# Kernel optimization log

Hardware: AMD Instinct MI355X
Metric: run time of the kernel (lower is better)

## Reference

```python
import jax, jax.numpy as jnp
import numpy as np

INPUT_SIZE = 256
HIDDEN_SIZE = 256


def _xavier(key, shape):
    fan_in, fan_out = shape
    limit = float(np.sqrt(6.0 / (fan_in + fan_out)))
    return jax.random.uniform(key, shape, jnp.float32, -limit, limit)


def setup_inputs() -> dict:
    key = jax.random.key(0)
    ks = jax.random.split(key, 9)
    X = jax.random.normal(ks[0], (64, 2048, INPUT_SIZE), jnp.float32)
    E, H = INPUT_SIZE, HIDDEN_SIZE
    return {
        "X": X,
        "W_ii": _xavier(ks[1], (E, H)), "W_hi": _xavier(ks[2], (H, H)), "b_i": jnp.zeros((H,), jnp.float32),
        "W_if": _xavier(ks[3], (E, H)), "W_hf": _xavier(ks[4], (H, H)), "b_f": jnp.zeros((H,), jnp.float32),
        "W_ig": _xavier(ks[5], (E, H)), "W_hg": _xavier(ks[6], (H, H)), "b_g": jnp.zeros((H,), jnp.float32),
        "W_io": _xavier(ks[7], (E, H)), "W_ho": _xavier(ks[8], (H, H)), "b_o": jnp.zeros((H,), jnp.float32),
    }


def reference(X, W_ii, W_hi, b_i, W_if, W_hf, b_f, W_ig, W_hg, b_g, W_io, W_ho, b_o):
    B, S, E = X.shape
    H = W_ii.shape[1]
    h0 = jnp.zeros((B, H), X.dtype)  # init state in torch code is zeros (broadcasts to (B,H))
    c0 = jnp.zeros((B, H), X.dtype)

    def step(carry, x_t):
        h, c = carry
        i = jax.nn.sigmoid(x_t @ W_ii + h @ W_hi + b_i)
        f = jax.nn.sigmoid(x_t @ W_if + h @ W_hf + b_f)
        g = jnp.tanh(x_t @ W_ig + h @ W_hg + b_g)
        o = jax.nn.sigmoid(x_t @ W_io + h @ W_ho + b_o)
        c = f * c + i * g
        h = o * jnp.tanh(c)
        return (h, c), h

    (h_t, c_t), hs = jax.lax.scan(step, (h0, c0), jnp.swapaxes(X, 0, 1))  # hs: (S,B,H)
    hiddenSeqs = jnp.swapaxes(hs, 0, 1)  # (B,S,H)
    return hiddenSeqs, (h_t, c_t)
```

## Files before the change

### kernel.cpp

```cpp
#include <hip/hip_runtime.h>

typedef _Float16 f16;
typedef _Float16 f16x2 __attribute__((ext_vector_type(2)));
typedef _Float16 f16x8 __attribute__((ext_vector_type(8)));
typedef float    f32x4 __attribute__((ext_vector_type(4)));
typedef unsigned int u32x4 __attribute__((ext_vector_type(4)));

#if defined(__has_builtin)
#if __has_builtin(__builtin_amdgcn_fdot2)
#define HAVE_FDOT2 1
#endif
#endif

#ifdef HAVE_FDOT2
#define FDOT2(a, b, c) __builtin_amdgcn_fdot2((a), (b), (c), false)
#else
static __device__ __forceinline__ float FDOT2(f16x2 a, f16x2 b, float c) {
  return c + (float)a[0] * (float)b[0] + (float)a[1] * (float)b[1];
}
#endif

static __device__ __forceinline__ f16x2 asf16x2(unsigned int v) {
  return __builtin_bit_cast(f16x2, v);
}

struct PtrPack { const float* p[8]; };

__global__ __launch_bounds__(256) void k_prep(PtrPack pp, f16* __restrict__ wxT,
                                              f16* __restrict__ whT) {
  int m = blockIdx.z, kt = blockIdx.y, ut = blockIdx.x;
  const float* src = pp.p[m];
  f16* dst = (m < 4) ? (wxT + m * 65536) : (whT + (m - 4) * 65536);
  __shared__ f16 tile[64][66];
  int c = threadIdx.x & 63, r0 = threadIdx.x >> 6;
#pragma unroll
  for (int i = 0; i < 16; ++i) {
    int r = i * 4 + r0;
    tile[c][r] = (f16)src[(kt * 64 + r) * 256 + ut * 64 + c];
  }
  __syncthreads();
#pragma unroll
  for (int i = 0; i < 16; ++i) {
    int ul = i * 4 + r0;
    dst[(size_t)(ut * 64 + ul) * 256 + kt * 64 + c] = tile[ul][c];
  }
}

__global__ __launch_bounds__(256) void k_gemm(const float* __restrict__ X,
                                              const f16* __restrict__ wxT,
                                              f16* __restrict__ xw, int chunk0) {
  int nblk = blockIdx.x;
  int mblk = blockIdx.y;
  int b    = blockIdx.z;
  __shared__ f16 Alds[64][48];
  __shared__ f16 Blds[256][48];
  int tid = threadIdx.x, wave = tid >> 6, lane = tid & 63;
  int l15 = lane & 15, l4 = lane >> 4;
  f32x4 acc[16];
#pragma unroll
  for (int i = 0; i < 16; ++i) acc[i] = (f32x4){0.f, 0.f, 0.f, 0.f};
  const float* Xb = X + ((size_t)b * 2048 + chunk0 + mblk * 64) * 256;
  const f16*   Bb = wxT + (size_t)nblk * 256 * 256;
  int arow = tid >> 2, akq = (tid & 3) * 8;

  for (int kk = 0; kk < 8; ++kk) {
    {
      const float* s = Xb + arow * 256 + kk * 32 + akq;
      float4 v0 = *(const float4*)s;
      float4 v1 = *(const float4*)(s + 4);
      union { f16 h[8]; uint4 q; } u;
      u.h[0] = (f16)v0.x; u.h[1] = (f16)v0.y; u.h[2] = (f16)v0.z; u.h[3] = (f16)v0.w;
      u.h[4] = (f16)v1.x; u.h[5] = (f16)v1.y; u.h[6] = (f16)v1.z; u.h[7] = (f16)v1.w;
      *(uint4*)(&Alds[arow][akq]) = u.q;
    }
    {
      const uint4* s = (const uint4*)(Bb + (size_t)tid * 256 + kk * 32);
      uint4* d = (uint4*)(&Blds[tid][0]);
      d[0] = s[0]; d[1] = s[1]; d[2] = s[2]; d[3] = s[3];
    }
    __syncthreads();
    f16x8 a = *(const f16x8*)(&Alds[wave * 16 + l15][l4 * 8]);
#pragma unroll
    for (int nt = 0; nt < 16; ++nt) {
      f16x8 bb = *(const f16x8*)(&Blds[nt * 16 + l15][l4 * 8]);
      acc[nt] = __builtin_amdgcn_mfma_f32_16x16x32_f16(a, bb, acc[nt], 0, 0, 0);
    }
    __syncthreads();
  }
#pragma unroll
  for (int nt = 0; nt < 16; ++nt) {
#pragma unroll
    for (int r = 0; r < 4; ++r) {
      int trow = mblk * 64 + wave * 16 + l4 * 4 + r;
      int col  = nblk * 256 + nt * 16 + l15;
      xw[((size_t)trow * 64 + b) * 1024 + col] = (f16)acc[nt][r];
    }
  }
}

__global__ __launch_bounds__(512, 2) void k_rnn(
    const f16* __restrict__ xw, const f16* __restrict__ whT,
    const float* __restrict__ bi, const float* __restrict__ bf_,
    const float* __restrict__ bg, const float* __restrict__ bo,
    float* __restrict__ out, float* __restrict__ hstate, float* __restrict__ cstate,
    int chunk0, int chunk_len) {
  extern __shared__ char smem[];
  u32x4* WO = (u32x4*)smem;
  float4* psum = (float4*)(smem + 131072);
  unsigned short* hb = (unsigned short*)(smem + 135168);
  int b = blockIdx.x;
  int u = threadIdx.x & 255;
  int half = threadIdx.x >> 8;

  const u32x4* wo = (const u32x4*)(whT + (size_t)(3 * 256 + u) * 256 + half * 128);
#pragma unroll
  for (int j = 0; j < 16; ++j) WO[(half * 16 + j) * 256 + u] = wo[j];

  const volatile u32x4* wi =
      (const volatile u32x4*)(whT + (size_t)(0 * 256 + u) * 256 + half * 128);
  const volatile u32x4* wf =
      (const volatile u32x4*)(whT + (size_t)(1 * 256 + u) * 256 + half * 128);
  const volatile u32x4* wg =
      (const volatile u32x4*)(whT + (size_t)(2 * 256 + u) * 256 + half * 128);
  u32x4 Wi[16], Wf[16], Wg[16];
#pragma unroll
  for (int j = 0; j < 16; ++j) { Wi[j] = wi[j]; Wf[j] = wf[j]; Wg[j] = wg[j]; }

  float B0 = bi[u], B1 = bf_[u], B2 = bg[u], B3 = bo[u];

  float c, h;
  if (chunk0 == 0) { c = 0.f; h = 0.f; }
  else { c = cstate[b * 256 + u]; h = hstate[b * 256 + u]; }
  if (!half) hb[u] = __builtin_bit_cast(unsigned short, (f16)h);
  __syncthreads();

  int p = 0;
#pragma unroll 1
  for (int t = 0; t < chunk_len; ++t) {
    float x0 = 0.f, x1 = 0.f, x2 = 0.f, x3 = 0.f;
    if (!half) {
      const f16* xwt = xw + ((size_t)t * 64 + b) * 1024 + u;
      x0 = (float)xwt[0]; x1 = (float)xwt[256]; x2 = (float)xwt[512]; x3 = (float)xwt[768];
    }
    const u32x4* hq = (const u32x4*)(hb + p * 256) + half * 16;
    float a0 = 0.f, a1 = 0.f, a2 = 0.f, a3 = 0.f;
#pragma unroll
    for (int j = 0; j < 16; ++j) {
      u32x4 h4 = hq[j];
      u32x4 w3 = WO[(half * 16 + j) * 256 + u];
      a0 = FDOT2(asf16x2(h4.x), asf16x2(Wi[j].x), a0);
      a1 = FDOT2(asf16x2(h4.x), asf16x2(Wf[j].x), a1);
      a2 = FDOT2(asf16x2(h4.x), asf16x2(Wg[j].x), a2);
      a3 = FDOT2(asf16x2(h4.x), asf16x2(w3.x), a3);
      a0 = FDOT2(asf16x2(h4.y), asf16x2(Wi[j].y), a0);
      a1 = FDOT2(asf16x2(h4.y), asf16x2(Wf[j].y), a1);
      a2 = FDOT2(asf16x2(h4.y), asf16x2(Wg[j].y), a2);
      a3 = FDOT2(asf16x2(h4.y), asf16x2(w3.y), a3);
      a0 = FDOT2(asf16x2(h4.z), asf16x2(Wi[j].z), a0);
      a1 = FDOT2(asf16x2(h4.z), asf16x2(Wf[j].z), a1);
      a2 = FDOT2(asf16x2(h4.z), asf16x2(Wg[j].z), a2);
      a3 = FDOT2(asf16x2(h4.z), asf16x2(w3.z), a3);
      a0 = FDOT2(asf16x2(h4.w), asf16x2(Wi[j].w), a0);
      a1 = FDOT2(asf16x2(h4.w), asf16x2(Wf[j].w), a1);
      a2 = FDOT2(asf16x2(h4.w), asf16x2(Wg[j].w), a2);
      a3 = FDOT2(asf16x2(h4.w), asf16x2(w3.w), a3);
    }
    if (half) {
      psum[u] = (float4){a0, a1, a2, a3};
    }
    __syncthreads();
    if (!half) {
      float4 ps = psum[u];
      a0 += ps.x + x0 + B0;
      a1 += ps.y + x1 + B1;
      a2 += ps.z + x2 + B2;
      a3 += ps.w + x3 + B3;
      float gi = 1.f / (1.f + __expf(-a0));
      float gf = 1.f / (1.f + __expf(-a1));
      float e2 = __expf(-2.f * fabsf(a2));
      float gg = copysignf((1.f - e2) / (1.f + e2), a2);
      float go = 1.f / (1.f + __expf(-a3));
      c = gf * c + gi * gg;
      float ec = __expf(-2.f * fabsf(c));
      float tc = copysignf((1.f - ec) / (1.f + ec), c);
      h = go * tc;
      int gt = chunk0 + t;
      out[((size_t)b * 2048 + gt) * 256 + u] = h;
      hb[(p ^ 1) * 256 + u] = __builtin_bit_cast(unsigned short, (f16)h);
      if (gt == 2047) {
        out[33554432 + b * 256 + u] = h;
        out[33554432 + 16384 + b * 256 + u] = c;
      }
    }
    __syncthreads();
    p ^= 1;
  }
  if ((chunk0 + chunk_len < 2048) && !half) {
    hstate[b * 256 + u] = h;
    cstate[b * 256 + u] = c;
  }
}

extern "C" void kernel_launch(void* const* d_in, const int* in_sizes, int n_in,
                              void* d_out, int out_size, void* d_ws, size_t ws_size,
                              hipStream_t stream) {
  const float* X = (const float*)d_in[0];
  PtrPack pp;
  pp.p[0] = (const float*)d_in[1];
  pp.p[1] = (const float*)d_in[4];
  pp.p[2] = (const float*)d_in[7];
  pp.p[3] = (const float*)d_in[10];
  pp.p[4] = (const float*)d_in[2];
  pp.p[5] = (const float*)d_in[5];
  pp.p[6] = (const float*)d_in[8];
  pp.p[7] = (const float*)d_in[11];
  const float* bi  = (const float*)d_in[3];
  const float* bf_ = (const float*)d_in[6];
  const float* bg  = (const float*)d_in[9];
  const float* bo  = (const float*)d_in[12];
  float* out = (float*)d_out;

  char* ws = (char*)d_ws;
  f16*   wxT    = (f16*)ws;
  f16*   whT    = (f16*)(ws + 524288);
  float* hstate = (float*)(ws + 1048576);
  float* cstate = (float*)(ws + 1114112);
  f16*   xwbuf  = (f16*)(ws + 1179648);

  long avail = (ws_size > 1310720) ? (long)(ws_size - 1310720) : 0;
  long sc = avail / 131072;
  sc = (sc / 64) * 64;
  if (sc < 64) sc = 64;
  if (sc > 2048) sc = 2048;

  static const int RNN_SMEM = 131072 + 4096 + 1024;
  hipFuncSetAttribute((const void*)k_rnn, hipFuncAttributeMaxDynamicSharedMemorySize,
                      RNN_SMEM);

  k_prep<<<dim3(4, 4, 8), 256, 0, stream>>>(pp, wxT, whT);

  for (int s0 = 0; s0 < 2048; s0 += (int)sc) {
    int len = (int)((2048 - s0) < sc ? (2048 - s0) : sc);
    k_gemm<<<dim3(4, len / 64, 64), 256, 0, stream>>>(X, wxT, xwbuf, s0);
    k_rnn<<<dim3(64), 512, RNN_SMEM, stream>>>(xwbuf, whT, bi, bf_, bg, bo, out,
                                               hstate, cstate, s0, len);
  }
}
```

Baseline: 3.326 ms.

## Stream input and forget gate recurrent weights from L2 instead of registers

Adds a prep kernel that stores the recurrent weights in an interleaved layout, so that each thread's 16-byte chunks for consecutive j are 256 elements apart and loads coalesce across threads. The recurrent kernel now keeps only the g-gate weights in registers and the o-gate weights in LDS. The i and f weights are reloaded from global memory (expected to hit L2) on every timestep. The goal is to cut register pressure and allow more occupancy or better scheduling, at the cost of two global loads per inner iteration on the serial critical path.

```diff
diff --git a/kernel.cpp b/kernel.cpp
--- a/kernel.cpp
+++ b/kernel.cpp
@@ -26,11 +26,10 @@
 
 struct PtrPack { const float* p[8]; };
 
-__global__ __launch_bounds__(256) void k_prep(PtrPack pp, f16* __restrict__ wxT,
-                                              f16* __restrict__ whT) {
+__global__ __launch_bounds__(256) void k_prep(PtrPack pp, f16* __restrict__ wxT) {
   int m = blockIdx.z, kt = blockIdx.y, ut = blockIdx.x;
   const float* src = pp.p[m];
-  f16* dst = (m < 4) ? (wxT + m * 65536) : (whT + (m - 4) * 65536);
+  f16* dst = wxT + m * 65536;
   __shared__ f16 tile[64][66];
   int c = threadIdx.x & 63, r0 = threadIdx.x >> 6;
 #pragma unroll
@@ -43,6 +42,23 @@
   for (int i = 0; i < 16; ++i) {
     int ul = i * 4 + r0;
     dst[(size_t)(ut * 64 + ul) * 256 + kt * 64 + c] = tile[ul][c];
+  }
+}
+
+__global__ __launch_bounds__(256) void k_prepI(PtrPack pp, u32x4* __restrict__ whI) {
+  int kb = blockIdx.x;
+  int m  = blockIdx.y;
+  const float* src = pp.p[4 + m];
+  int u = threadIdx.x;
+  f16 v[64];
+#pragma unroll
+  for (int kk = 0; kk < 64; ++kk) v[kk] = (f16)src[(size_t)(kb * 64 + kk) * 256 + u];
+#pragma unroll
+  for (int cc = 0; cc < 8; ++cc) {
+    union { f16 h[8]; u32x4 q; } pk;
+#pragma unroll
+    for (int e = 0; e < 8; ++e) pk.h[e] = v[cc * 8 + e];
+    whI[(size_t)m * 8192 + (size_t)(kb * 8 + cc) * 256 + u] = pk.q;
   }
 }
 
@@ -99,7 +115,7 @@
 }
 
 __global__ __launch_bounds__(512, 2) void k_rnn(
-    const f16* __restrict__ xw, const f16* __restrict__ whT,
+    const f16* __restrict__ xw, const u32x4* __restrict__ whI,
     const float* __restrict__ bi, const float* __restrict__ bf_,
     const float* __restrict__ bg, const float* __restrict__ bo,
     float* __restrict__ out, float* __restrict__ hstate, float* __restrict__ cstate,
@@ -111,20 +127,17 @@
   int b = blockIdx.x;
   int u = threadIdx.x & 255;
   int half = threadIdx.x >> 8;
-
-  const u32x4* wo = (const u32x4*)(whT + (size_t)(3 * 256 + u) * 256 + half * 128);
-#pragma unroll
-  for (int j = 0; j < 16; ++j) WO[(half * 16 + j) * 256 + u] = wo[j];
-
-  const volatile u32x4* wi =
-      (const volatile u32x4*)(whT + (size_t)(0 * 256 + u) * 256 + half * 128);
-  const volatile u32x4* wf =
-      (const volatile u32x4*)(whT + (size_t)(1 * 256 + u) * 256 + half * 128);
-  const volatile u32x4* wg =
-      (const volatile u32x4*)(whT + (size_t)(2 * 256 + u) * 256 + half * 128);
-  u32x4 Wi[16], Wf[16], Wg[16];
-#pragma unroll
-  for (int j = 0; j < 16; ++j) { Wi[j] = wi[j]; Wf[j] = wf[j]; Wg[j] = wg[j]; }
+  int base = (half * 16) * 256 + u;
+
+#pragma unroll
+  for (int j = 0; j < 16; ++j) WO[base + j * 256] = whI[3 * 8192 + base + j * 256];
+
+  u32x4 Wg[16];
+#pragma unroll
+  for (int j = 0; j < 16; ++j) {
+    Wg[j] = whI[2 * 8192 + base + j * 256];
+    asm volatile("" : "+v"(Wg[j]));
+  }
 
   float B0 = bi[u], B1 = bf_[u], B2 = bg[u], B3 = bo[u];
 
@@ -133,6 +146,9 @@
   else { c = cstate[b * 256 + u]; h = hstate[b * 256 + u]; }
   if (!half) hb[u] = __builtin_bit_cast(unsigned short, (f16)h);
   __syncthreads();
+
+  const u32x4* wIi = whI + base;
+  const u32x4* wIf = whI + 8192 + base;
 
   int p = 0;
 #pragma unroll 1
@@ -146,24 +162,26 @@
     float a0 = 0.f, a1 = 0.f, a2 = 0.f, a3 = 0.f;
 #pragma unroll
     for (int j = 0; j < 16; ++j) {
-      u32x4 h4 = hq[j];
-      u32x4 w3 = WO[(half * 16 + j) * 256 + u];
-      a0 = FDOT2(asf16x2(h4.x), asf16x2(Wi[j].x), a0);
-      a1 = FDOT2(asf16x2(h4.x), asf16x2(Wf[j].x), a1);
+      u32x4 wi_ = wIi[j * 256];
+      u32x4 wf_ = wIf[j * 256];
+      u32x4 h4  = hq[j];
+      u32x4 wo_ = WO[base + j * 256];
+      a0 = FDOT2(asf16x2(h4.x), asf16x2(wi_.x), a0);
+      a1 = FDOT2(asf16x2(h4.x), asf16x2(wf_.x), a1);
       a2 = FDOT2(asf16x2(h4.x), asf16x2(Wg[j].x), a2);
-      a3 = FDOT2(asf16x2(h4.x), asf16x2(w3.x), a3);
-      a0 = FDOT2(asf16x2(h4.y), asf16x2(Wi[j].y), a0);
-      a1 = FDOT2(asf16x2(h4.y), asf16x2(Wf[j].y), a1);
+      a3 = FDOT2(asf16x2(h4.x), asf16x2(wo_.x), a3);
+      a0 = FDOT2(asf16x2(h4.y), asf16x2(wi_.y), a0);
+      a1 = FDOT2(asf16x2(h4.y), asf16x2(wf_.y), a1);
       a2 = FDOT2(asf16x2(h4.y), asf16x2(Wg[j].y), a2);
-      a3 = FDOT2(asf16x2(h4.y), asf16x2(w3.y), a3);
-      a0 = FDOT2(asf16x2(h4.z), asf16x2(Wi[j].z), a0);
-      a1 = FDOT2(asf16x2(h4.z), asf16x2(Wf[j].z), a1);
+      a3 = FDOT2(asf16x2(h4.y), asf16x2(wo_.y), a3);
+      a0 = FDOT2(asf16x2(h4.z), asf16x2(wi_.z), a0);
+      a1 = FDOT2(asf16x2(h4.z), asf16x2(wf_.z), a1);
       a2 = FDOT2(asf16x2(h4.z), asf16x2(Wg[j].z), a2);
-      a3 = FDOT2(asf16x2(h4.z), asf16x2(w3.z), a3);
-      a0 = FDOT2(asf16x2(h4.w), asf16x2(Wi[j].w), a0);
-      a1 = FDOT2(asf16x2(h4.w), asf16x2(Wf[j].w), a1);
+      a3 = FDOT2(asf16x2(h4.z), asf16x2(wo_.z), a3);
+      a0 = FDOT2(asf16x2(h4.w), asf16x2(wi_.w), a0);
+      a1 = FDOT2(asf16x2(h4.w), asf16x2(wf_.w), a1);
       a2 = FDOT2(asf16x2(h4.w), asf16x2(Wg[j].w), a2);
-      a3 = FDOT2(asf16x2(h4.w), asf16x2(w3.w), a3);
+      a3 = FDOT2(asf16x2(h4.w), asf16x2(wo_.w), a3);
     }
     if (half) {
       psum[u] = (float4){a0, a1, a2, a3};
@@ -222,7 +240,7 @@
 
   char* ws = (char*)d_ws;
   f16*   wxT    = (f16*)ws;
-  f16*   whT    = (f16*)(ws + 524288);
+  u32x4* whI    = (u32x4*)(ws + 524288);
   float* hstate = (float*)(ws + 1048576);
   float* cstate = (float*)(ws + 1114112);
   f16*   xwbuf  = (f16*)(ws + 1179648);
@@ -237,12 +255,13 @@
   hipFuncSetAttribute((const void*)k_rnn, hipFuncAttributeMaxDynamicSharedMemorySize,
                       RNN_SMEM);
 
-  k_prep<<<dim3(4, 4, 8), 256, 0, stream>>>(pp, wxT, whT);
+  k_prep<<<dim3(4, 4, 4), 256, 0, stream>>>(pp, wxT);
+  k_prepI<<<dim3(4, 4), 256, 0, stream>>>(pp, whI);
 
   for (int s0 = 0; s0 < 2048; s0 += (int)sc) {
     int len = (int)((2048 - s0) < sc ? (2048 - s0) : sc);
     k_gemm<<<dim3(4, len / 64, 64), 256, 0, stream>>>(X, wxT, xwbuf, s0);
-    k_rnn<<<dim3(64), 512, RNN_SMEM, stream>>>(xwbuf, whT, bi, bf_, bg, bo, out,
+    k_rnn<<<dim3(64), 512, RNN_SMEM, stream>>>(xwbuf, whI, bi, bf_, bg, bo, out,
                                                hstate, cstate, s0, len);
   }
 }
```

Result: no change. 3.353 ms (+0.8%).
